# Kernel tuning notes

Measured on AMD Instinct MI355X. Metric: run time of the kernel, lower is better.

## Reference

```python
import jax, jax.numpy as jnp
import numpy as np

B = 16384
IN = 128
H = 128
NC = 10
NATT = 3
EPS = 1e-5


def setup_inputs() -> dict:
    key = jax.random.key(0)
    ks = jax.random.split(key, 8)
    s_in = 1.0 / np.sqrt(IN)
    s_h = 1.0 / np.sqrt(H)
    return {
        "x": jax.random.normal(ks[0], (B, IN), dtype=jnp.float32),
        "W_in": jax.random.uniform(ks[1], (IN, H), jnp.float32, -s_in, s_in),
        "b_in": jax.random.uniform(ks[2], (H,), jnp.float32, -s_in, s_in),
        "W_att": jax.random.uniform(ks[3], (NATT, H, H), jnp.float32, -s_h, s_h),
        "b_att": jax.random.uniform(ks[4], (NATT, H), jnp.float32, -s_h, s_h),
        "gamma": jnp.ones((NATT, H), jnp.float32),
        "beta": jnp.zeros((NATT, H), jnp.float32),
        "W_c": jax.random.uniform(ks[5], (H, NC), jnp.float32, -s_h, s_h),
        "b_c": jax.random.uniform(ks[6], (NC,), jnp.float32, -s_h, s_h),
    }


def _layernorm(y, g, b):
    mu = jnp.mean(y, axis=-1, keepdims=True)
    var = jnp.mean((y - mu) ** 2, axis=-1, keepdims=True)
    return (y - mu) * jax.lax.rsqrt(var + EPS) * g + b


def reference(x, W_in, b_in, W_att, b_att, gamma, beta, W_c, b_c):
    # in_proj: [B, IN] -> [B, H]
    h = x @ W_in + b_in
    for i in range(NATT):
        u = jnp.tanh(h @ W_att[i] + b_att[i])            # [B, H]
        scores = u[:, :, None] * u[:, None, :]            # outer product [B, H, H]
        attn = jax.nn.softmax(scores, axis=-1)
        out = jnp.einsum("bij,bj->bi", attn, h)          # [B, H]
        h = _layernorm(h + out, gamma[i], beta[i])
    return h @ W_c + b_c                                  # [B, NC]
```

## Files before the change

kernel.cpp:

```cpp
#include <hip/hip_runtime.h>
#include <math.h>

#define B_TOT 16384
#define H     128
#define NC    10
#define NATT  3
#define TR    16
#define HBS   136
#define KT    5
#define EPS   1e-5f

typedef __attribute__((ext_vector_type(8))) short bf16x8;
typedef __attribute__((ext_vector_type(4))) float f32x4;

__device__ __forceinline__ ushort f2bf(float f) {
    union { float f; unsigned u; } v; v.f = f;
    unsigned r = v.u + 0x7fffu + ((v.u >> 16) & 1u);
    return (ushort)(r >> 16);
}

__device__ __forceinline__ float fast_tanh(float a) {
    a = fminf(15.f, fmaxf(-15.f, a));
    float t = __expf(2.f * a);
    return (t - 1.f) / (t + 1.f);
}

template<int CTRL>
__device__ __forceinline__ float dpp_add(float v) {
    int x = __float_as_int(v);
    int y = __builtin_amdgcn_update_dpp(0, x, CTRL, 0xf, 0xf, false);
    return v + __int_as_float(y);
}
__device__ __forceinline__ float red16(float v) {
    v = dpp_add<0x121>(v);
    v = dpp_add<0x122>(v);
    v = dpp_add<0x124>(v);
    v = dpp_add<0x128>(v);
    return v;
}

extern "C" __global__ __launch_bounds__(256)
void prep_weights(const float* __restrict__ W_in,
                  const float* __restrict__ W_att,
                  const float* __restrict__ W_c,
                  ushort* __restrict__ wt)
{
    int i = blockIdx.x * 256 + threadIdx.x;
    if (i < 65536) {
        int mat = i >> 14, idx = i & 16383;
        int k = idx >> 7, n = idx & 127;
        float v = (mat == 0) ? W_in[idx] : W_att[(mat - 1) * 16384 + idx];
        wt[mat * 16384 + n * H + k] = f2bf(v);
    } else if (i < 65536 + 2048) {
        int idx = i - 65536;
        int n = idx >> 7, k = idx & 127;
        float v = (n < NC) ? W_c[k * NC + n] : 0.f;
        wt[65536 + n * H + k] = f2bf(v);
    }
}

extern "C" __global__ __launch_bounds__(64, 1)
void simple_attention_kernel(const float* __restrict__ x,
                             const float* __restrict__ b_in,
                             const float* __restrict__ b_att,
                             const float* __restrict__ gamma,
                             const float* __restrict__ beta,
                             const float* __restrict__ b_c,
                             const ushort* __restrict__ wt,
                             float* __restrict__ out)
{
    __shared__ __align__(16) ushort ab[TR * HBS];

    const int lane = threadIdx.x;
    const int s    = lane & 15;
    const int q    = lane >> 4;
    const size_t rowBase = (size_t)blockIdx.x * TR;

    float h[8][4];
    f32x4 acc[8];

    {
        bf16x8 af[4];
        #pragma unroll
        for (int ks = 0; ks < 4; ++ks) {
            const float* xp = x + (rowBase + s) * H + ks * 32 + q * 8;
            float4 v0 = *(const float4*)xp;
            float4 v1 = *(const float4*)(xp + 4);
            bf16x8 a;
            a[0] = f2bf(v0.x); a[1] = f2bf(v0.y); a[2] = f2bf(v0.z); a[3] = f2bf(v0.w);
            a[4] = f2bf(v1.x); a[5] = f2bf(v1.y); a[6] = f2bf(v1.z); a[7] = f2bf(v1.w);
            af[ks] = a;
        }
        #pragma unroll
        for (int t = 0; t < 8; ++t) acc[t] = (f32x4){0.f, 0.f, 0.f, 0.f};
        #pragma unroll
        for (int ks = 0; ks < 4; ++ks) {
            #pragma unroll
            for (int t = 0; t < 8; ++t) {
                bf16x8 b = *(const bf16x8*)&wt[(16 * t + s) * H + ks * 32 + q * 8];
                acc[t] = __builtin_amdgcn_mfma_f32_16x16x32_bf16(af[ks], b, acc[t], 0, 0, 0);
            }
        }
        #pragma unroll
        for (int t = 0; t < 8; ++t) {
            float bi = b_in[16 * t + s];
            #pragma unroll
            for (int r = 0; r < 4; ++r) {
                h[t][r] = acc[t][r] + bi;
                ab[(4 * q + r) * HBS + 16 * t + s] = f2bf(h[t][r]);
            }
        }
    }

    const float cm[KT] = {1.00004478f, 0.99730768f, 0.49919676f, 0.17734736f, 0.04379392f};

    #pragma unroll 1
    for (int layer = 0; layer < NATT; ++layer) {
        const ushort* WT = wt + (size_t)(1 + layer) * 16384;

        bf16x8 af[4];
        #pragma unroll
        for (int ks = 0; ks < 4; ++ks)
            af[ks] = *(const bf16x8*)&ab[s * HBS + ks * 32 + q * 8];
        #pragma unroll
        for (int t = 0; t < 8; ++t) acc[t] = (f32x4){0.f, 0.f, 0.f, 0.f};
        #pragma unroll
        for (int ks = 0; ks < 4; ++ks) {
            #pragma unroll
            for (int t = 0; t < 8; ++t) {
                bf16x8 b = *(const bf16x8*)&WT[(16 * t + s) * H + ks * 32 + q * 8];
                acc[t] = __builtin_amdgcn_mfma_f32_16x16x32_bf16(af[ks], b, acc[t], 0, 0, 0);
            }
        }
        float u[8][4];
        #pragma unroll
        for (int t = 0; t < 8; ++t) {
            float ba = b_att[layer * H + 16 * t + s];
            #pragma unroll
            for (int r = 0; r < 4; ++r) u[t][r] = fast_tanh(acc[t][r] + ba);
        }

        float S[4][KT], T[4][KT - 1];
        #pragma unroll
        for (int r = 0; r < 4; ++r) {
            #pragma unroll
            for (int k = 0; k < KT; ++k) S[r][k] = 0.f;
            #pragma unroll
            for (int k = 0; k < KT - 1; ++k) T[r][k] = 0.f;
        }
        #pragma unroll
        for (int t = 0; t < 8; ++t) {
            #pragma unroll
            for (int r = 0; r < 4; ++r) {
                float uu = u[t][r], hh = h[t][r];
                S[r][0] += hh;
                float p = uu;
                S[r][1] += p * hh; T[r][0] += p;
                #pragma unroll
                for (int k = 2; k < KT; ++k) {
                    p *= uu;
                    S[r][k] += p * hh;
                    T[r][k - 1] += p;
                }
            }
        }
        #pragma unroll
        for (int r = 0; r < 4; ++r) {
            #pragma unroll
            for (int k = 0; k < KT; ++k)     S[r][k] = red16(S[r][k]) * cm[k];
            #pragma unroll
            for (int k = 0; k < KT - 1; ++k) T[r][k] = red16(T[r][k]) * cm[k + 1];
        }

        float ls[4] = {0,0,0,0}, lq[4] = {0,0,0,0};
        #pragma unroll
        for (int t = 0; t < 8; ++t) {
            #pragma unroll
            for (int r = 0; r < 4; ++r) {
                float uu = u[t][r];
                float num = S[r][KT - 1];
                #pragma unroll
                for (int k = KT - 2; k >= 0; --k) num = num * uu + S[r][k];
                float den = T[r][KT - 2];
                #pragma unroll
                for (int k = KT - 3; k >= 0; --k) den = den * uu + T[r][k];
                den = den * uu + 128.f * 1.00004478f;
                float yy = h[t][r] + num * __builtin_amdgcn_rcpf(den);
                h[t][r] = yy;
                ls[r] += yy; lq[r] += yy * yy;
            }
        }
        #pragma unroll
        for (int r = 0; r < 4; ++r) { ls[r] = red16(ls[r]); lq[r] = red16(lq[r]); }
        float mu[4], inv[4];
        #pragma unroll
        for (int r = 0; r < 4; ++r) {
            mu[r] = ls[r] * (1.f / H);
            float var = lq[r] * (1.f / H) - mu[r] * mu[r];
            inv[r] = rsqrtf(var + EPS);
        }
        #pragma unroll
        for (int t = 0; t < 8; ++t) {
            int n = 16 * t + s;
            float g  = gamma[layer * H + n];
            float be = beta [layer * H + n];
            #pragma unroll
            for (int r = 0; r < 4; ++r) {
                float hn = (h[t][r] - mu[r]) * inv[r] * g + be;
                h[t][r] = hn;
                ab[(4 * q + r) * HBS + n] = f2bf(hn);
            }
        }
    }

    {
        const ushort* WC = wt + 4 * 16384;
        f32x4 facc = (f32x4){0.f, 0.f, 0.f, 0.f};
        #pragma unroll
        for (int ks = 0; ks < 4; ++ks) {
            bf16x8 a = *(const bf16x8*)&ab[s * HBS + ks * 32 + q * 8];
            bf16x8 b = *(const bf16x8*)&WC[s * H + ks * 32 + q * 8];
            facc = __builtin_amdgcn_mfma_f32_16x16x32_bf16(a, b, facc, 0, 0, 0);
        }
        if (s < NC) {
            float bc = b_c[s];
            #pragma unroll
            for (int r = 0; r < 4; ++r)
                out[(rowBase + 4 * q + r) * NC + s] = facc[r] + bc;
        }
    }
}

extern "C" void kernel_launch(void* const* d_in, const int* in_sizes, int n_in,
                              void* d_out, int out_size, void* d_ws, size_t ws_size,
                              hipStream_t stream) {
    const float* x     = (const float*)d_in[0];
    const float* W_in  = (const float*)d_in[1];
    const float* b_in  = (const float*)d_in[2];
    const float* W_att = (const float*)d_in[3];
    const float* b_att = (const float*)d_in[4];
    const float* gamma = (const float*)d_in[5];
    const float* beta  = (const float*)d_in[6];
    const float* W_c   = (const float*)d_in[7];
    const float* b_c   = (const float*)d_in[8];
    float* out  = (float*)d_out;
    ushort* wt  = (ushort*)d_ws;

    hipLaunchKernelGGL(prep_weights, dim3(264), dim3(256), 0, stream,
                       W_in, W_att, W_c, wt);
    hipLaunchKernelGGL(simple_attention_kernel, dim3(B_TOT / TR), dim3(64), 0, stream,
                       x, b_in, b_att, gamma, beta, b_c, wt, out);
}
```

Baseline: 102.7 us.

## Split hidden columns across two wavefronts per block with LDS partial-sum exchange

Each 16-row block now runs two wavefronts, and each one owns 64 of the 128 hidden columns. This halves the per-thread register state and the MFMA/elementwise work per wave. The partial polynomial-attention sums and the layernorm statistics are exchanged through shared memory, with added __syncthreads barriers. The aim is more parallelism and occupancy per row tile, at the cost of extra LDS traffic and synchronisation. In the final classifier step only wave 0 does any work.

```diff
diff --git a/kernel.cpp b/kernel.cpp
--- a/kernel.cpp
+++ b/kernel.cpp
@@ -59,7 +59,7 @@
     }
 }
 
-extern "C" __global__ __launch_bounds__(64, 1)
+extern "C" __global__ __launch_bounds__(128, 2)
 void simple_attention_kernel(const float* __restrict__ x,
                              const float* __restrict__ b_in,
                              const float* __restrict__ b_att,
@@ -70,14 +70,18 @@
                              float* __restrict__ out)
 {
     __shared__ __align__(16) ushort ab[TR * HBS];
-
-    const int lane = threadIdx.x;
+    __shared__ __align__(16) float  exm[2 * 16 * 12];
+    __shared__ __align__(16) float  exl[2 * 16 * 2];
+
+    const int tid  = threadIdx.x;
+    const int wv   = tid >> 6;
+    const int lane = tid & 63;
     const int s    = lane & 15;
     const int q    = lane >> 4;
     const size_t rowBase = (size_t)blockIdx.x * TR;
 
-    float h[8][4];
-    f32x4 acc[8];
+    float h[4][4];
+    f32x4 acc[4];
 
     {
         bf16x8 af[4];
@@ -92,24 +96,26 @@
             af[ks] = a;
         }
         #pragma unroll
-        for (int t = 0; t < 8; ++t) acc[t] = (f32x4){0.f, 0.f, 0.f, 0.f};
-        #pragma unroll
-        for (int ks = 0; ks < 4; ++ks) {
-            #pragma unroll
-            for (int t = 0; t < 8; ++t) {
-                bf16x8 b = *(const bf16x8*)&wt[(16 * t + s) * H + ks * 32 + q * 8];
+        for (int t = 0; t < 4; ++t) acc[t] = (f32x4){0.f, 0.f, 0.f, 0.f};
+        #pragma unroll
+        for (int ks = 0; ks < 4; ++ks) {
+            #pragma unroll
+            for (int t = 0; t < 4; ++t) {
+                bf16x8 b = *(const bf16x8*)&wt[(64 * wv + 16 * t + s) * H + ks * 32 + q * 8];
                 acc[t] = __builtin_amdgcn_mfma_f32_16x16x32_bf16(af[ks], b, acc[t], 0, 0, 0);
             }
         }
         #pragma unroll
-        for (int t = 0; t < 8; ++t) {
-            float bi = b_in[16 * t + s];
+        for (int t = 0; t < 4; ++t) {
+            int n = 64 * wv + 16 * t + s;
+            float bi = b_in[n];
             #pragma unroll
             for (int r = 0; r < 4; ++r) {
                 h[t][r] = acc[t][r] + bi;
-                ab[(4 * q + r) * HBS + 16 * t + s] = f2bf(h[t][r]);
-            }
-        }
+                ab[(4 * q + r) * HBS + n] = f2bf(h[t][r]);
+            }
+        }
+        __syncthreads();
     }
 
     const float cm[KT] = {1.00004478f, 0.99730768f, 0.49919676f, 0.17734736f, 0.04379392f};
@@ -123,19 +129,19 @@
         for (int ks = 0; ks < 4; ++ks)
             af[ks] = *(const bf16x8*)&ab[s * HBS + ks * 32 + q * 8];
         #pragma unroll
-        for (int t = 0; t < 8; ++t) acc[t] = (f32x4){0.f, 0.f, 0.f, 0.f};
-        #pragma unroll
-        for (int ks = 0; ks < 4; ++ks) {
-            #pragma unroll
-            for (int t = 0; t < 8; ++t) {
-                bf16x8 b = *(const bf16x8*)&WT[(16 * t + s) * H + ks * 32 + q * 8];
+        for (int t = 0; t < 4; ++t) acc[t] = (f32x4){0.f, 0.f, 0.f, 0.f};
+        #pragma unroll
+        for (int ks = 0; ks < 4; ++ks) {
+            #pragma unroll
+            for (int t = 0; t < 4; ++t) {
+                bf16x8 b = *(const bf16x8*)&WT[(64 * wv + 16 * t + s) * H + ks * 32 + q * 8];
                 acc[t] = __builtin_amdgcn_mfma_f32_16x16x32_bf16(af[ks], b, acc[t], 0, 0, 0);
             }
         }
-        float u[8][4];
-        #pragma unroll
-        for (int t = 0; t < 8; ++t) {
-            float ba = b_att[layer * H + 16 * t + s];
+        float u[4][4];
+        #pragma unroll
+        for (int t = 0; t < 4; ++t) {
+            float ba = b_att[layer * H + 64 * wv + 16 * t + s];
             #pragma unroll
             for (int r = 0; r < 4; ++r) u[t][r] = fast_tanh(acc[t][r] + ba);
         }
@@ -149,7 +155,7 @@
             for (int k = 0; k < KT - 1; ++k) T[r][k] = 0.f;
         }
         #pragma unroll
-        for (int t = 0; t < 8; ++t) {
+        for (int t = 0; t < 4; ++t) {
             #pragma unroll
             for (int r = 0; r < 4; ++r) {
                 float uu = u[t][r], hh = h[t][r];
@@ -167,14 +173,40 @@
         #pragma unroll
         for (int r = 0; r < 4; ++r) {
             #pragma unroll
-            for (int k = 0; k < KT; ++k)     S[r][k] = red16(S[r][k]) * cm[k];
-            #pragma unroll
-            for (int k = 0; k < KT - 1; ++k) T[r][k] = red16(T[r][k]) * cm[k + 1];
+            for (int k = 0; k < KT; ++k)     S[r][k] = red16(S[r][k]);
+            #pragma unroll
+            for (int k = 0; k < KT - 1; ++k) T[r][k] = red16(T[r][k]);
+        }
+        if (s == 0) {
+            #pragma unroll
+            for (int r = 0; r < 4; ++r) {
+                float* dst = &exm[(wv * 16 + 4 * q + r) * 12];
+                *(f32x4*)&dst[0] = (f32x4){S[r][0], S[r][1], S[r][2], S[r][3]};
+                *(f32x4*)&dst[4] = (f32x4){S[r][4], T[r][0], T[r][1], T[r][2]};
+                dst[8] = T[r][3];
+            }
+        }
+        __syncthreads();
+        #pragma unroll
+        for (int r = 0; r < 4; ++r) {
+            const float* src = &exm[((1 - wv) * 16 + 4 * q + r) * 12];
+            f32x4 c0 = *(const f32x4*)&src[0];
+            f32x4 c1 = *(const f32x4*)&src[4];
+            float c2 = src[8];
+            S[r][0] = (S[r][0] + c0.x) * cm[0];
+            S[r][1] = (S[r][1] + c0.y) * cm[1];
+            S[r][2] = (S[r][2] + c0.z) * cm[2];
+            S[r][3] = (S[r][3] + c0.w) * cm[3];
+            S[r][4] = (S[r][4] + c1.x) * cm[4];
+            T[r][0] = (T[r][0] + c1.y) * cm[1];
+            T[r][1] = (T[r][1] + c1.z) * cm[2];
+            T[r][2] = (T[r][2] + c1.w) * cm[3];
+            T[r][3] = (T[r][3] + c2)   * cm[4];
         }
 
         float ls[4] = {0,0,0,0}, lq[4] = {0,0,0,0};
         #pragma unroll
-        for (int t = 0; t < 8; ++t) {
+        for (int t = 0; t < 4; ++t) {
             #pragma unroll
             for (int r = 0; r < 4; ++r) {
                 float uu = u[t][r];
@@ -192,16 +224,24 @@
         }
         #pragma unroll
         for (int r = 0; r < 4; ++r) { ls[r] = red16(ls[r]); lq[r] = red16(lq[r]); }
+        if (s == 0) {
+            #pragma unroll
+            for (int r = 0; r < 4; ++r)
+                *(float2*)&exl[(wv * 16 + 4 * q + r) * 2] = make_float2(ls[r], lq[r]);
+        }
+        __syncthreads();
         float mu[4], inv[4];
         #pragma unroll
         for (int r = 0; r < 4; ++r) {
-            mu[r] = ls[r] * (1.f / H);
-            float var = lq[r] * (1.f / H) - mu[r] * mu[r];
+            float2 o = *(const float2*)&exl[((1 - wv) * 16 + 4 * q + r) * 2];
+            float sm = ls[r] + o.x, sq = lq[r] + o.y;
+            mu[r] = sm * (1.f / H);
+            float var = sq * (1.f / H) - mu[r] * mu[r];
             inv[r] = rsqrtf(var + EPS);
         }
         #pragma unroll
-        for (int t = 0; t < 8; ++t) {
-            int n = 16 * t + s;
+        for (int t = 0; t < 4; ++t) {
+            int n = 64 * wv + 16 * t + s;
             float g  = gamma[layer * H + n];
             float be = beta [layer * H + n];
             #pragma unroll
@@ -211,9 +251,10 @@
                 ab[(4 * q + r) * HBS + n] = f2bf(hn);
             }
         }
-    }
-
-    {
+        __syncthreads();
+    }
+
+    if (wv == 0) {
         const ushort* WC = wt + 4 * 16384;
         f32x4 facc = (f32x4){0.f, 0.f, 0.f, 0.f};
         #pragma unroll
@@ -248,6 +289,6 @@
 
     hipLaunchKernelGGL(prep_weights, dim3(264), dim3(256), 0, stream,
                        W_in, W_att, W_c, wt);
-    hipLaunchKernelGGL(simple_attention_kernel, dim3(B_TOT / TR), dim3(64), 0, stream,
+    hipLaunchKernelGGL(simple_attention_kernel, dim3(B_TOT / TR), dim3(128), 0, stream,
                        x, b_in, b_att, gamma, beta, b_c, wt, out);
 }
```

Result: no change. 101.8 us (-0.9%).
